# Performance work log

Hardware: AMD Instinct MI355X
Metric: run time of the kernel (lower is better)

The kernel has to match this reference:

```python
import jax, jax.numpy as jnp
import numpy as np

V = 4096   # input_dim (one-hot / vocab size)
H = 256    # hidden_dim
O = 512    # output_dim
B = 64     # batch
T = 512    # sequence length


def setup_inputs() -> dict:
    key = jax.random.key(0)
    ks = jax.random.split(key, 7)
    s = 1.0 / np.sqrt(H)  # PyTorch nn.RNN / nn.Linear init range
    x = jax.random.randint(ks[0], (B, T), 0, V)
    W_ih = jax.random.uniform(ks[1], (H, V), minval=-s, maxval=s, dtype=jnp.float32)
    W_hh = jax.random.uniform(ks[2], (H, H), minval=-s, maxval=s, dtype=jnp.float32)
    b_ih = jax.random.uniform(ks[3], (H,), minval=-s, maxval=s, dtype=jnp.float32)
    b_hh = jax.random.uniform(ks[4], (H,), minval=-s, maxval=s, dtype=jnp.float32)
    W_fc = jax.random.uniform(ks[5], (O, H), minval=-s, maxval=s, dtype=jnp.float32)
    b_fc = jax.random.uniform(ks[6], (O,), minval=-s, maxval=s, dtype=jnp.float32)
    return {"x": x, "W_ih": W_ih, "W_hh": W_hh, "b_ih": b_ih, "b_hh": b_hh,
            "W_fc": W_fc, "b_fc": b_fc}


def reference(x, W_ih, W_hh, b_ih, b_hh, W_fc, b_fc):
    # one_hot(x, V).float() @ W_ih.T is algebraically a row-gather of W_ih.T
    x_proj = jnp.take(W_ih.T, x, axis=0) + b_ih  # [B, T, H]

    def step(h, xt):
        h = jnp.tanh(xt + h @ W_hh.T + b_hh)  # vanilla tanh RNN cell
        return h, h

    h0 = jnp.zeros((x.shape[0], W_hh.shape[0]), dtype=x_proj.dtype)
    _, hs = jax.lax.scan(step, h0, jnp.swapaxes(x_proj, 0, 1))  # [T, B, H]
    hs = jnp.swapaxes(hs, 0, 1)  # [B, T, H]
    return hs @ W_fc.T + b_fc  # [B, T, O]
```

## Files before the change

### kernel.cpp

```cpp
#include <hip/hip_runtime.h>

#define V 4096
#define H 256
#define O 512
#define B 64
#define T 512

typedef __attribute__((ext_vector_type(8))) short bf16x8;
typedef __attribute__((ext_vector_type(4))) float f32x4;
typedef __attribute__((ext_vector_type(2))) float f32x2;

__device__ __forceinline__ unsigned short f2bf(float f) {
    unsigned int u = __float_as_uint(f);
    u += 0x7fffu + ((u >> 16) & 1u);
    return (unsigned short)(u >> 16);
}
__device__ __forceinline__ float bf2f(unsigned short s) {
    return __uint_as_float(((unsigned int)s) << 16);
}

__device__ __forceinline__ float dpp_xor1(float v) {
    int i = __float_as_int(v);
    return __int_as_float(__builtin_amdgcn_update_dpp(i, i, 0xB1, 0xf, 0xf, true));
}
__device__ __forceinline__ float dpp_xor2(float v) {
    int i = __float_as_int(v);
    return __int_as_float(__builtin_amdgcn_update_dpp(i, i, 0x4E, 0xf, 0xf, true));
}
__device__ __forceinline__ float dpp_ror4(float v) {
    int i = __float_as_int(v);
    return __int_as_float(__builtin_amdgcn_update_dpp(i, i, 0x124, 0xf, 0xf, true));
}
__device__ __forceinline__ float dpp_ror8(float v) {
    int i = __float_as_int(v);
    return __int_as_float(__builtin_amdgcn_update_dpp(i, i, 0x128, 0xf, 0xf, true));
}

__global__ __launch_bounds__(256) void k_transpose(const float* __restrict__ Wih,
                                                   float* __restrict__ WihT) {
    __shared__ float tile[64][65];
    const int bi = blockIdx.x & 3;
    const int bv = blockIdx.x >> 2;
    const int tx = threadIdx.x & 63, ty = threadIdx.x >> 6;
#pragma unroll
    for (int s = 0; s < 16; ++s) {
        int r = ty + 4 * s;
        tile[r][tx] = Wih[(size_t)(bi * 64 + r) * V + bv * 64 + tx];
    }
    __syncthreads();
#pragma unroll
    for (int s = 0; s < 16; ++s) {
        int r = ty + 4 * s;
        WihT[(size_t)(bv * 64 + r) * H + bi * 64 + tx] = tile[tx][r];
    }
}

__global__ __launch_bounds__(256) void k_prep(const float* __restrict__ Wfc,
                                              unsigned short* __restrict__ hi,
                                              unsigned short* __restrict__ lo) {
    int i = blockIdx.x * 256 + threadIdx.x;
    float w = Wfc[i];
    unsigned short h = f2bf(w);
    hi[i] = h;
    lo[i] = f2bf(w - bf2f(h));
}

#define CH16 20

__global__ __launch_bounds__(512, 2) void k_rnn(
    const int* __restrict__ x, const float* __restrict__ WihT,
    const float* __restrict__ Whh, const float* __restrict__ b_ih,
    const float* __restrict__ b_hh,
    unsigned short* __restrict__ hs_hi) {
    __shared__ float hsm[2][16 * CH16];
    const int b = blockIdx.x;
    const int tid = threadIdx.x;
    const int c = tid & 15;
    const int g = tid >> 4;
    const int row = 8 * g + (c & 7);
    const int k0 = 16 * c;

    f32x2 w2[8][8];
#pragma unroll
    for (int r = 0; r < 8; ++r) {
        const f32x2* wr = (const f32x2*)(Whh + (size_t)(8 * g + r) * H + k0);
#pragma unroll
        for (int q = 0; q < 8; ++q) w2[r][q] = wr[q];
    }

    if (tid < 16 * CH16) hsm[0][tid] = 0.0f;
    const float bias = b_ih[row] + b_hh[row];
    __syncthreads();

    const int bT = b * T;
    int x0 = x[bT];
    int xt1 = x[bT + 1];
    float xp_cur = WihT[(size_t)x0 * H + row];

    for (int t = 0; t < T; ++t) {
        float xp_next = WihT[(size_t)xt1 * H + row];

        const f32x4* hv = (const f32x4*)&hsm[t & 1][c * CH16];
        f32x4 q0 = hv[0], q1 = hv[1], q2 = hv[2], q3 = hv[3];
        f32x2 h2[8] = {{q0[0], q0[1]}, {q0[2], q0[3]}, {q1[0], q1[1]}, {q1[2], q1[3]},
                       {q2[0], q2[1]}, {q2[2], q2[3]}, {q3[0], q3[1]}, {q3[2], q3[3]}};
        f32x2 a0 = {0,0}, a1 = {0,0}, a2 = {0,0}, a3 = {0,0};
        f32x2 a4 = {0,0}, a5 = {0,0}, a6 = {0,0}, a7 = {0,0};
#pragma unroll
        for (int q = 0; q < 8; ++q) {
            a0 += h2[q] * w2[0][q];
            a1 += h2[q] * w2[1][q];
            a2 += h2[q] * w2[2][q];
            a3 += h2[q] * w2[3][q];
            a4 += h2[q] * w2[4][q];
            a5 += h2[q] * w2[5][q];
            a6 += h2[q] * w2[6][q];
            a7 += h2[q] * w2[7][q];
        }
        float s0 = a0[0] + a0[1], s1 = a1[0] + a1[1];
        float s2 = a2[0] + a2[1], s3 = a3[0] + a3[1];
        float s4 = a4[0] + a4[1], s5 = a5[0] + a5[1];
        float s6 = a6[0] + a6[1], s7 = a7[0] + a7[1];
        s0 += dpp_xor1(s0); s1 += dpp_xor1(s1); s2 += dpp_xor1(s2); s3 += dpp_xor1(s3);
        s4 += dpp_xor1(s4); s5 += dpp_xor1(s5); s6 += dpp_xor1(s6); s7 += dpp_xor1(s7);
        const bool b0 = c & 1, b1 = c & 2, b2 = c & 4;
        float u0 = b0 ? s1 : s0;
        float u1 = b0 ? s3 : s2;
        float u2 = b0 ? s5 : s4;
        float u3 = b0 ? s7 : s6;
        u0 += dpp_xor2(u0); u1 += dpp_xor2(u1); u2 += dpp_xor2(u2); u3 += dpp_xor2(u3);
        float v0 = b1 ? u1 : u0;
        float v1 = b1 ? u3 : u2;
        v0 += dpp_ror4(v0); v1 += dpp_ror4(v1);
        v0 += dpp_ror8(v0); v1 += dpp_ror8(v1);
        float own = b2 ? v1 : v0;

        float pre = own + xp_cur + bias;
        float e = __expf(2.0f * pre);
        float hval = 1.0f - 2.0f * __builtin_amdgcn_rcpf(e + 1.0f);

        if (c < 8)
            hsm[(t + 1) & 1][(row >> 4) * CH16 + (row & 15)] = hval;

        asm volatile("s_waitcnt lgkmcnt(0)" ::: "memory");
        __builtin_amdgcn_s_barrier();

        if (c < 8)
            __builtin_nontemporal_store(
                f2bf(hval), &hs_hi[(size_t)(bT + t) * H + row]);
        xp_cur = xp_next;
        int tnn = (t + 2 < T) ? t + 2 : T - 1;
        xt1 = x[bT + tnn];
    }
}

__global__ __launch_bounds__(256, 2) void k_fc(
    const unsigned short* __restrict__ hs_hi,
    const unsigned short* __restrict__ wfc_hi, const unsigned short* __restrict__ wfc_lo,
    const float* __restrict__ b_fc, float* __restrict__ out) {
    __shared__ short sA[128 * 64], sBh[128 * 64], sBl[128 * 64];
    const int tid = threadIdx.x;
    const int bm = blockIdx.x >> 2, bn = blockIdx.x & 3;
    const int m0 = bm * 128, n0 = bn * 128;
    const int w = tid >> 6, lane = tid & 63;
    const int wm = w >> 1, wn = w & 1;
    const int l16 = lane & 15, g = lane >> 4;

    f32x4 acc[4][4];
#pragma unroll
    for (int a = 0; a < 4; ++a)
#pragma unroll
        for (int cc = 0; cc < 4; ++cc)
#pragma unroll
            for (int qq = 0; qq < 4; ++qq) acc[a][cc][qq] = 0.0f;

    for (int kt = 0; kt < 4; ++kt) {
        const int k0 = kt * 64;
#pragma unroll
        for (int s = 0; s < 4; ++s) {
            int cidx = tid + 256 * s;
            int r = cidx >> 3, slot = cidx & 7;
            int dst = r * 64 + ((slot ^ (r & 7)) << 3);
            size_t ga = (size_t)(m0 + r) * 256 + k0 + slot * 8;
            *(bf16x8*)&sA[dst] = *(const bf16x8*)&hs_hi[ga];
            size_t gb = (size_t)(n0 + r) * 256 + k0 + slot * 8;
            *(bf16x8*)&sBh[dst] = *(const bf16x8*)&wfc_hi[gb];
            *(bf16x8*)&sBl[dst] = *(const bf16x8*)&wfc_lo[gb];
        }
        __syncthreads();
#pragma unroll
        for (int kc = 0; kc < 2; ++kc) {
            bf16x8 ah[4], bh[4], bl[4];
            const int slot = kc * 4 + g;
#pragma unroll
            for (int mi = 0; mi < 4; ++mi) {
                int r = wm * 64 + mi * 16 + l16;
                int off = r * 64 + ((slot ^ (r & 7)) << 3);
                ah[mi] = *(const bf16x8*)&sA[off];
            }
#pragma unroll
            for (int ni = 0; ni < 4; ++ni) {
                int r = wn * 64 + ni * 16 + l16;
                int off = r * 64 + ((slot ^ (r & 7)) << 3);
                bh[ni] = *(const bf16x8*)&sBh[off];
                bl[ni] = *(const bf16x8*)&sBl[off];
            }
#pragma unroll
            for (int mi = 0; mi < 4; ++mi)
#pragma unroll
                for (int ni = 0; ni < 4; ++ni) {
                    acc[mi][ni] = __builtin_amdgcn_mfma_f32_16x16x32_bf16(
                        ah[mi], bh[ni], acc[mi][ni], 0, 0, 0);
                    acc[mi][ni] = __builtin_amdgcn_mfma_f32_16x16x32_bf16(
                        ah[mi], bl[ni], acc[mi][ni], 0, 0, 0);
                }
        }
        __syncthreads();
    }
#pragma unroll
    for (int ni = 0; ni < 4; ++ni) {
        int n = n0 + wn * 64 + ni * 16 + l16;
        float bfc = b_fc[n];
#pragma unroll
        for (int mi = 0; mi < 4; ++mi) {
#pragma unroll
            for (int qq = 0; qq < 4; ++qq) {
                int m = m0 + wm * 64 + mi * 16 + g * 4 + qq;
                out[(size_t)m * O + n] = acc[mi][ni][qq] + bfc;
            }
        }
    }
}

extern "C" void kernel_launch(void* const* d_in, const int* in_sizes, int n_in,
                              void* d_out, int out_size, void* d_ws, size_t ws_size,
                              hipStream_t stream) {
    (void)in_sizes; (void)n_in; (void)out_size; (void)ws_size;
    const int*   x    = (const int*)d_in[0];
    const float* Wih  = (const float*)d_in[1];
    const float* Whh  = (const float*)d_in[2];
    const float* bih  = (const float*)d_in[3];
    const float* bhh  = (const float*)d_in[4];
    const float* Wfc  = (const float*)d_in[5];
    const float* bfc  = (const float*)d_in[6];
    float* out = (float*)d_out;

    char* ws = (char*)d_ws;
    float*          WihT = (float*)ws;
    unsigned short* wfch = (unsigned short*)(ws + 4194304);
    unsigned short* wfcl = (unsigned short*)(ws + 4194304 + 262144);
    unsigned short* hsh  = (unsigned short*)(ws + 4718592);

    k_transpose<<<256, 256, 0, stream>>>(Wih, WihT);
    k_prep<<<512, 256, 0, stream>>>(Wfc, wfch, wfcl);
    k_rnn<<<64, 512, 0, stream>>>(x, WihT, Whh, bih, bhh, hsh);
    k_fc<<<1024, 256, 0, stream>>>(hsh, wfch, wfcl, bfc, out);
}
```

Baseline: 361.2 us.

## Split RNN recurrence K-dimension across 32 lanes with 1024-thread blocks

The recurrent matvec now uses 1024 threads per batch block. Each thread covers 8 K-elements instead of 16, halving per-thread FMA work and register weights on the serial critical path. The cross-lane reduction gains a permlane32 swap stage to combine the two wave halves. The bf16 store switches to a hardware pack instruction. The cost is a larger block barrier across 16 waves and one extra reduction step per timestep.

```diff
diff --git a/kernel.cpp b/kernel.cpp
--- a/kernel.cpp
+++ b/kernel.cpp
@@ -34,6 +34,11 @@
 __device__ __forceinline__ float dpp_ror8(float v) {
     int i = __float_as_int(v);
     return __int_as_float(__builtin_amdgcn_update_dpp(i, i, 0x128, 0xf, 0xf, true));
+}
+__device__ __forceinline__ float xor32_add(float x) {
+    float y = x;
+    asm("v_permlane32_swap_b32 %0, %1" : "+v"(y), "+v"(x));
+    return x + y;
 }
 
 __global__ __launch_bounds__(256) void k_transpose(const float* __restrict__ Wih,
@@ -65,57 +70,57 @@
     lo[i] = f2bf(w - bf2f(h));
 }
 
-#define CH16 20
-
-__global__ __launch_bounds__(512, 2) void k_rnn(
+#define CHS 12
+
+__global__ __launch_bounds__(1024) void k_rnn(
     const int* __restrict__ x, const float* __restrict__ WihT,
     const float* __restrict__ Whh, const float* __restrict__ b_ih,
     const float* __restrict__ b_hh,
     unsigned short* __restrict__ hs_hi) {
-    __shared__ float hsm[2][16 * CH16];
+    __shared__ float hsm[2][32 * CHS];
     const int b = blockIdx.x;
     const int tid = threadIdx.x;
-    const int c = tid & 15;
-    const int g = tid >> 4;
-    const int row = 8 * g + (c & 7);
-    const int k0 = 16 * c;
-
-    f32x2 w2[8][8];
+    const int lane = tid & 63;
+    const int wave = tid >> 6;
+    const int kk = (lane & 15) | ((lane & 32) >> 1);
+    const int g = ((lane >> 4) & 1) | (wave << 1);
+    const int own_row = 8 * g + (kk & 7);
+    const int k0 = 8 * kk;
+
+    f32x2 w2[8][4];
 #pragma unroll
     for (int r = 0; r < 8; ++r) {
         const f32x2* wr = (const f32x2*)(Whh + (size_t)(8 * g + r) * H + k0);
 #pragma unroll
-        for (int q = 0; q < 8; ++q) w2[r][q] = wr[q];
-    }
-
-    if (tid < 16 * CH16) hsm[0][tid] = 0.0f;
-    const float bias = b_ih[row] + b_hh[row];
+        for (int j = 0; j < 4; ++j) w2[r][j] = wr[j];
+    }
+
+    if (tid < 32 * CHS) hsm[0][tid] = 0.0f;
+    const float bias = b_ih[own_row] + b_hh[own_row];
     __syncthreads();
 
     const int bT = b * T;
-    int x0 = x[bT];
-    int xt1 = x[bT + 1];
-    float xp_cur = WihT[(size_t)x0 * H + row];
+    float xp_cur = WihT[(size_t)x[bT] * H + own_row];
+    int xnext = x[bT + 1];
 
     for (int t = 0; t < T; ++t) {
-        float xp_next = WihT[(size_t)xt1 * H + row];
-
-        const f32x4* hv = (const f32x4*)&hsm[t & 1][c * CH16];
-        f32x4 q0 = hv[0], q1 = hv[1], q2 = hv[2], q3 = hv[3];
-        f32x2 h2[8] = {{q0[0], q0[1]}, {q0[2], q0[3]}, {q1[0], q1[1]}, {q1[2], q1[3]},
-                       {q2[0], q2[1]}, {q2[2], q2[3]}, {q3[0], q3[1]}, {q3[2], q3[3]}};
+        float xp_next = WihT[(size_t)xnext * H + own_row];
+
+        const f32x4* hv = (const f32x4*)&hsm[t & 1][kk * CHS];
+        f32x4 q0 = hv[0], q1 = hv[1];
+        f32x2 h2[4] = {{q0[0], q0[1]}, {q0[2], q0[3]}, {q1[0], q1[1]}, {q1[2], q1[3]}};
         f32x2 a0 = {0,0}, a1 = {0,0}, a2 = {0,0}, a3 = {0,0};
         f32x2 a4 = {0,0}, a5 = {0,0}, a6 = {0,0}, a7 = {0,0};
 #pragma unroll
-        for (int q = 0; q < 8; ++q) {
-            a0 += h2[q] * w2[0][q];
-            a1 += h2[q] * w2[1][q];
-            a2 += h2[q] * w2[2][q];
-            a3 += h2[q] * w2[3][q];
-            a4 += h2[q] * w2[4][q];
-            a5 += h2[q] * w2[5][q];
-            a6 += h2[q] * w2[6][q];
-            a7 += h2[q] * w2[7][q];
+        for (int j = 0; j < 4; ++j) {
+            a0 += h2[j] * w2[0][j];
+            a1 += h2[j] * w2[1][j];
+            a2 += h2[j] * w2[2][j];
+            a3 += h2[j] * w2[3][j];
+            a4 += h2[j] * w2[4][j];
+            a5 += h2[j] * w2[5][j];
+            a6 += h2[j] * w2[6][j];
+            a7 += h2[j] * w2[7][j];
         }
         float s0 = a0[0] + a0[1], s1 = a1[0] + a1[1];
         float s2 = a2[0] + a2[1], s3 = a3[0] + a3[1];
@@ -123,7 +128,7 @@
         float s6 = a6[0] + a6[1], s7 = a7[0] + a7[1];
         s0 += dpp_xor1(s0); s1 += dpp_xor1(s1); s2 += dpp_xor1(s2); s3 += dpp_xor1(s3);
         s4 += dpp_xor1(s4); s5 += dpp_xor1(s5); s6 += dpp_xor1(s6); s7 += dpp_xor1(s7);
-        const bool b0 = c & 1, b1 = c & 2, b2 = c & 4;
+        const bool b0 = kk & 1, b1 = kk & 2, b2 = kk & 4;
         float u0 = b0 ? s1 : s0;
         float u1 = b0 ? s3 : s2;
         float u2 = b0 ? s5 : s4;
@@ -133,24 +138,29 @@
         float v1 = b1 ? u3 : u2;
         v0 += dpp_ror4(v0); v1 += dpp_ror4(v1);
         v0 += dpp_ror8(v0); v1 += dpp_ror8(v1);
+        v0 = xor32_add(v0);
+        v1 = xor32_add(v1);
         float own = b2 ? v1 : v0;
 
         float pre = own + xp_cur + bias;
         float e = __expf(2.0f * pre);
         float hval = 1.0f - 2.0f * __builtin_amdgcn_rcpf(e + 1.0f);
 
-        if (c < 8)
-            hsm[(t + 1) & 1][(row >> 4) * CH16 + (row & 15)] = hval;
+        if ((kk & 24) == 8)
+            hsm[(t + 1) & 1][g * CHS + (kk & 7)] = hval;
+
+        int hb;
+        asm("v_cvt_pk_bf16_f32 %0, %1, %2" : "=v"(hb) : "v"(hval), "v"(0.0f));
 
         asm volatile("s_waitcnt lgkmcnt(0)" ::: "memory");
         __builtin_amdgcn_s_barrier();
 
-        if (c < 8)
-            __builtin_nontemporal_store(
-                f2bf(hval), &hs_hi[(size_t)(bT + t) * H + row]);
+        if ((kk & 24) == 0)
+            __builtin_nontemporal_store((unsigned short)hb,
+                                        &hs_hi[(size_t)(bT + t) * H + own_row]);
         xp_cur = xp_next;
         int tnn = (t + 2 < T) ? t + 2 : T - 1;
-        xt1 = x[bT + tnn];
+        xnext = x[bT + tnn];
     }
 }
 
@@ -253,6 +263,6 @@
 
     k_transpose<<<256, 256, 0, stream>>>(Wih, WihT);
     k_prep<<<512, 256, 0, stream>>>(Wfc, wfch, wfcl);
-    k_rnn<<<64, 512, 0, stream>>>(x, WihT, Whh, bih, bhh, hsh);
+    k_rnn<<<64, 1024, 0, stream>>>(x, WihT, Whh, bih, bhh, hsh);
     k_fc<<<1024, 256, 0, stream>>>(hsh, wfch, wfcl, bfc, out);
 }
```

Measured after the change: 444.0 us. +22.9%, slower.
